# Kernel optimization log

Hardware: AMD Instinct MI355X
Metric: run time of the kernel (lower is better)

## Reference

```python
import jax, jax.numpy as jnp
import numpy as np


def setup_inputs() -> dict:
    key = jax.random.key(0)
    k1, k2 = jax.random.split(key)
    IN, OUT, N = 4096, 4096, 8192
    x = jax.random.normal(k1, (N, IN), dtype=jnp.float32)
    fc = jnp.arange(OUT, dtype=jnp.float32).reshape(-1, 1)  # learned param, init = arange
    bias = jax.random.normal(k2, (OUT,), dtype=jnp.float32) * 0.5
    return {"x": x, "fc": fc, "bias": bias}


def _dst_matrix(fc, in_features, dtype):
    out_features = fc.shape[0]
    t = jnp.arange(in_features, dtype=dtype)[None, :]          # [1, in]
    # torch.eye(out, 1): column vector, 1 at row 0 else 0
    eye_col = jnp.zeros((out_features, 1), dtype=dtype).at[0, 0].set(1.0)
    norm = jax.lax.rsqrt(2.0 * in_features * (eye_col + 1.0))  # [out, 1]
    # dst_m[k, t] = 2 * norm[k] * sin(pi/2 * (k+1)/in * (2t+1))
    dst_m = 2.0 * norm * jnp.sin(0.5 * jnp.pi * ((fc + 1.0) / in_features) * (2.0 * t + 1.0))
    return dst_m  # [out, in]


def reference(x, fc, bias):
    in_features = x.shape[-1]
    w = _dst_matrix(fc, in_features, x.dtype)  # [out, in]
    # F.linear: y = x @ w.T + bias
    return jnp.einsum('ni,oi->no', x, w) + bias
```

## Files before the change

### kernel.cpp

```cpp
#include <hip/hip_runtime.h>
#include <cstdint>
#include <cstddef>

#define IN_F 4096
#define OUT_F 4096
#define NROWS 8192
#define PI_F 3.14159265358979323846f

#define PD(a) ((a) + ((a) >> 4) + 3 * ((a) >> 7))
#define ROWSTR 2224

__device__ inline float2 cmul(float2 a, float2 b) {
    return make_float2(a.x * b.x - a.y * b.y, a.x * b.y + a.y * b.x);
}

__global__ void twprep(float2* __restrict__ tw, float2* __restrict__ f3,
                       float2* __restrict__ f23) {
    const int i = blockIdx.x * 256 + threadIdx.x;
    float s, c;
    if (i < 1024) {
        sincosf(-PI_F * (float)i / 1024.0f, &s, &c);
        tw[i] = make_float2(c, s);
    }
    sincosf(-PI_F * (float)i / 8192.0f, &s, &c);
    f3[i] = make_float2(c, s);
    sincosf(-PI_F * 5.0f * (float)i / 8192.0f, &s, &c);
    f23[i] = make_float2(c, s);
}

struct c4 { float2 z0, z1, z2, z3; };
__device__ __forceinline__ c4 r4unit(float2 x0, float2 x1, float2 x2, float2 x3) {
    const float2 E = make_float2(x0.x + x2.x, x0.y + x2.y);
    const float2 G = make_float2(x0.x - x2.x, x0.y - x2.y);
    const float2 F = make_float2(x1.x + x3.x, x1.y + x3.y);
    const float2 H = make_float2(x1.x - x3.x, x1.y - x3.y);
    c4 r;
    r.z0 = make_float2(E.x + F.x, E.y + F.y);
    r.z2 = make_float2(E.x - F.x, E.y - F.y);
    r.z1 = make_float2(G.x + H.y, G.y - H.x);
    r.z3 = make_float2(G.x - H.y, G.y + H.x);
    return r;
}

template<int S>
__device__ __forceinline__ void dif4(float2* __restrict__ V, int t,
                                     float2 u1, float2 u2) {
    const int h = 512 >> (2 * S);
    const int i = t & (h - 1);
    const int base = ((t >> (9 - 2 * S)) << (11 - 2 * S)) + i;
    const float2 u3 = cmul(u1, u2);
    const int p0 = PD(base), p1 = PD(base + h), p2 = PD(base + 2 * h),
              p3 = PD(base + 3 * h);
    const c4 r = r4unit(V[p0], V[p1], V[p2], V[p3]);
    V[p0] = r.z0;
    V[p1] = cmul(u1, r.z1);
    V[p2] = cmul(u2, r.z2);
    V[p3] = cmul(u3, r.z3);
}

#define WFENCE do { \
    asm volatile("s_waitcnt lgkmcnt(0)" ::: "memory"); \
    __builtin_amdgcn_sched_barrier(0); \
} while (0)

__global__ __launch_bounds__(512, 6) void dst_row(const float* __restrict__ x,
                                                  const float* __restrict__ bias,
                                                  const float2* __restrict__ twg,
                                                  const float2* __restrict__ f3,
                                                  const float2* __restrict__ f23,
                                                  float* __restrict__ out) {
    __shared__ float2 VV[2][ROWSTR];
    const int t = threadIdx.x;
    const int row0 = blockIdx.x * 2;
    const float* xr0 = x + (size_t)row0 * IN_F;
    const float* xr1 = xr0 + IN_F;
    float2* VA = VV[0];
    float2* VB = VV[1];

    const float2 w1 = twg[t];
    const float2 w2 = twg[2 * t];
    const float2 s1u1 = twg[(t & 127) << 2];
    const float2 s1u2 = twg[(t & 127) << 3];
    const float2 s2u1 = twg[(t & 31) << 4];
    const float2 s2u2 = twg[(t & 31) << 5];
    const float2 s3u1 = twg[(t & 7) << 6];
    const float2 s3u2 = twg[(t & 7) << 7];
    const float2 s4u1 = twg[(t & 1) << 8];
    const float2 s4u2 = twg[(t & 1) << 9];

    {
        const float2 w3 = cmul(w1, w2);
        {
            const float4 v0 = *(const float4*)(xr0 + 4 * t);
            const float4 v1 = *(const float4*)(xr0 + 4 * (t + 512));
            const float4 v2 = *(const float4*)(xr0 + (4092 - 4 * t));
            const float4 v3 = *(const float4*)(xr0 + (2044 - 4 * t));
            const c4 r = r4unit(make_float2(v0.x, v0.z), make_float2(v1.x, v1.z),
                                make_float2(-v2.w, -v2.y), make_float2(-v3.w, -v3.y));
            VA[PD(t)]        = r.z0;
            VA[PD(t + 512)]  = cmul(w1, r.z1);
            VA[PD(t + 1024)] = cmul(w2, r.z2);
            VA[PD(t + 1536)] = cmul(w3, r.z3);
        }
        {
            const float4 v0 = *(const float4*)(xr1 + 4 * t);
            const float4 v1 = *(const float4*)(xr1 + 4 * (t + 512));
            const float4 v2 = *(const float4*)(xr1 + (4092 - 4 * t));
            const float4 v3 = *(const float4*)(xr1 + (2044 - 4 * t));
            const c4 r = r4unit(make_float2(v0.x, v0.z), make_float2(v1.x, v1.z),
                                make_float2(-v2.w, -v2.y), make_float2(-v3.w, -v3.y));
            VB[PD(t)]        = r.z0;
            VB[PD(t + 512)]  = cmul(w1, r.z1);
            VB[PD(t + 1024)] = cmul(w2, r.z2);
            VB[PD(t + 1536)] = cmul(w3, r.z3);
        }
    }
    __syncthreads();

    dif4<1>(VA, t, s1u1, s1u2);
    dif4<1>(VB, t, s1u1, s1u2);
    __syncthreads();

    dif4<2>(VA, t, s2u1, s2u2);
    dif4<2>(VB, t, s2u1, s2u2);
    WFENCE;
    dif4<3>(VA, t, s3u1, s3u2);
    dif4<3>(VB, t, s3u1, s3u2);
    WFENCE;
    dif4<4>(VA, t, s4u1, s4u2);
    dif4<4>(VB, t, s4u1, s4u2);
    __syncthreads();

    const int rr = t >> 8;
    const int u = t & 255;
    const float2* V = VV[rr];
    float* yr = out + (size_t)(row0 + rr) * OUT_F;
    const float amp1 = 2.0f * rsqrtf(8192.0f);
    const float amp0 = 2.0f * rsqrtf(16384.0f);
#pragma unroll
    for (int q = 0; q < 8; ++q) {
        const int k = u + (q << 8);
        const int P = ((k & 3) << 9) | (((k >> 2) & 3) << 7) | (((k >> 4) & 3) << 5)
                    | (((k >> 6) & 3) << 3) | (((k >> 8) & 3) << 1);
        const float2 a = V[PD(P)];
        const float2 b = V[PD(P) + 1];
        const float2 z = (k < 1024) ? make_float2(a.x + b.x, a.y + b.y)
                                    : make_float2(a.x - b.x, a.y - b.y);
        const int kc = (2048 - k) & 2047;
        const int Pc = ((kc & 3) << 9) | (((kc >> 2) & 3) << 7) | (((kc >> 4) & 3) << 5)
                     | (((kc >> 6) & 3) << 3) | (((kc >> 8) & 3) << 1);
        const float2 ac = V[PD(Pc)];
        const float2 bc = V[PD(Pc) + 1];
        const float2 zc = (kc < 1024) ? make_float2(ac.x + bc.x, ac.y + bc.y)
                                      : make_float2(ac.x - bc.x, ac.y - bc.y);
        const float Arr = 0.5f * (z.x + zc.x), Aii = 0.5f * (z.y - zc.y);
        const float Brr = 0.5f * (z.y + zc.y), Bii = 0.5f * (zc.x - z.x);
        const float2 e3 = f3[k];
        const float2 eA = f23[k];
        const float Wr = Arr * e3.x - Aii * e3.y + Brr * eA.x - Bii * eA.y;
        const float Wi = Arr * e3.y + Aii * e3.x + Brr * eA.y + Bii * eA.x;
        const int o1 = 4095 - k;
        yr[o1] = amp1 * Wr + bias[o1];
        if (k > 0) {
            const int o2 = k - 1;
            const float amp = (o2 == 0) ? amp0 : amp1;
            yr[o2] = amp * (-Wi) + bias[o2];
        } else {
            const float C2048 = (z.x - z.y) * 0.70710678118654752f;
            yr[2047] = amp1 * C2048 + bias[2047];
        }
    }
}

__global__ __launch_bounds__(256) void dst_row_fb(const float* __restrict__ x,
                                                  const float* __restrict__ bias,
                                                  float* __restrict__ out) {
    __shared__ float Ar[2048], Ai[2048], Br[2048], Bi[2048];
    const int t = threadIdx.x;
    const int row = blockIdx.x;
    const float* xr = x + (size_t)row * IN_F;
    float* yr = out + (size_t)row * OUT_F;
#pragma unroll
    for (int q = 0; q < 8; ++q) {
        const int m = t + q * 256;
        float re, im;
        if (m < 1024) {
            const float4 v = *(const float4*)(xr + 4 * m);
            re = v.x; im = v.z;
        } else {
            const float4 v = *(const float4*)(xr + (8188 - 4 * m));
            re = -v.w; im = -v.y;
        }
        Ar[m] = re; Ai[m] = im;
    }
    __syncthreads();
    float *sr = Ar, *si = Ai, *dr = Br, *di = Bi;
    for (int s = 0; s < 11; ++s) {
        const int mm = 1024 >> s;
#pragma unroll
        for (int q = 0; q < 4; ++q) {
            const int b = t + q * 256;
            const int j = b >> (10 - s);
            const int i = b & (mm - 1);
            const int i0 = i + j * 2 * mm;
            const float ar = sr[i0], aim = si[i0];
            const float cr = sr[i0 + mm], ci = si[i0 + mm];
            float sw, cw;
            __sincosf(-PI_F * (float)j / (float)(1 << s), &sw, &cw);
            const float wr = cr * cw - ci * sw;
            const float wi = cr * sw + ci * cw;
            const int o0 = i + j * mm;
            dr[o0] = ar + wr;        di[o0] = aim + wi;
            dr[o0 + 1024] = ar - wr; di[o0 + 1024] = aim - wi;
        }
        __syncthreads();
        float* tp;
        tp = sr; sr = dr; dr = tp;
        tp = si; si = di; di = tp;
    }
    const float amp1 = 2.0f * rsqrtf(8192.0f);
    const float amp0 = 2.0f * rsqrtf(16384.0f);
#pragma unroll
    for (int q = 0; q < 8; ++q) {
        const int k = t + q * 256;
        const float zr = sr[k], zi = si[k];
        const int kc = (2048 - k) & 2047;
        const float cr = sr[kc], ci = si[kc];
        const float Arr = 0.5f * (zr + cr), Aii = 0.5f * (zi - ci);
        const float Brr = 0.5f * (zi + ci), Bii = 0.5f * (cr - zr);
        float s2, c2;
        __sincosf(-PI_F * (float)k / 2048.0f, &s2, &c2);
        const float Vr = Arr + Brr * c2 - Bii * s2;
        const float Vi = Aii + Brr * s2 + Bii * c2;
        float s3, c3;
        __sincosf(-PI_F * (float)k / 8192.0f, &s3, &c3);
        const float Wr = Vr * c3 - Vi * s3;
        const float Wi = Vr * s3 + Vi * c3;
        const int o1 = 4095 - k;
        yr[o1] = amp1 * Wr + bias[o1];
        if (k > 0) {
            const int o2 = k - 1;
            const float amp = (o2 == 0) ? amp0 : amp1;
            yr[o2] = amp * (-Wi) + bias[o2];
        } else {
            const float C2048 = (zr - zi) * 0.70710678118654752f;
            yr[2047] = amp1 * C2048 + bias[2047];
        }
    }
}

extern "C" void kernel_launch(void* const* d_in, const int* in_sizes, int n_in,
                              void* d_out, int out_size, void* d_ws, size_t ws_size,
                              hipStream_t stream) {
    const float* x    = (const float*)d_in[0];
    const float* bias = (const float*)d_in[2];
    float* out = (float*)d_out;

    if (ws_size >= 40960) {
        float2* tw  = (float2*)d_ws;
        float2* f3  = (float2*)((char*)d_ws + 8192);
        float2* f23 = (float2*)((char*)d_ws + 24576);
        twprep<<<8, 256, 0, stream>>>(tw, f3, f23);
        dst_row<<<NROWS / 2, 512, 0, stream>>>(x, bias, tw, f3, f23, out);
    } else {
        dst_row_fb<<<NROWS, 256, 0, stream>>>(x, bias, out);
    }
}
```

Baseline: 89.65 us.

## Assign one wavefront per row FFT, removing block-wide barriers between stages

Restructures the DST kernel so each 64-lane wavefront handles a whole 4096-point row (4 rows per 256-thread block). Every FFT stage then needs only a wavefront-local LDS wait instead of __syncthreads, and twiddles are staged once per block into shared memory rather than held in registers per thread. Each lane now does 8x more butterflies per stage, which lengthens the serial work per wave and may cut the number of loads in flight per row. It also changes occupancy through new launch bounds and a larger LDS footprint.

```diff
diff --git a/kernel.cpp b/kernel.cpp
--- a/kernel.cpp
+++ b/kernel.cpp
@@ -42,104 +42,88 @@
     return r;
 }
 
-template<int S>
-__device__ __forceinline__ void dif4(float2* __restrict__ V, int t,
-                                     float2 u1, float2 u2) {
-    const int h = 512 >> (2 * S);
-    const int i = t & (h - 1);
-    const int base = ((t >> (9 - 2 * S)) << (11 - 2 * S)) + i;
-    const float2 u3 = cmul(u1, u2);
-    const int p0 = PD(base), p1 = PD(base + h), p2 = PD(base + 2 * h),
-              p3 = PD(base + 3 * h);
-    const c4 r = r4unit(V[p0], V[p1], V[p2], V[p3]);
-    V[p0] = r.z0;
-    V[p1] = cmul(u1, r.z1);
-    V[p2] = cmul(u2, r.z2);
-    V[p3] = cmul(u3, r.z3);
-}
-
 #define WFENCE do { \
     asm volatile("s_waitcnt lgkmcnt(0)" ::: "memory"); \
     __builtin_amdgcn_sched_barrier(0); \
 } while (0)
 
-__global__ __launch_bounds__(512, 6) void dst_row(const float* __restrict__ x,
+template<int S>
+__device__ __forceinline__ void dif4w(float2* __restrict__ V,
+                                      const float2* __restrict__ TW, int lane) {
+#pragma unroll
+    for (int q = 0; q < 8; ++q) {
+        const int b = q * 64 + lane;
+        const int h = 512 >> (2 * S);
+        const int i = b & (h - 1);
+        const int base = ((b >> (9 - 2 * S)) << (11 - 2 * S)) + i;
+        const float2 u1 = TW[i << (2 * S)];
+        const float2 u2 = TW[i << (2 * S + 1)];
+        const float2 u3 = cmul(u1, u2);
+        const int p0 = PD(base), p1 = PD(base + h), p2 = PD(base + 2 * h),
+                  p3 = PD(base + 3 * h);
+        const c4 r = r4unit(V[p0], V[p1], V[p2], V[p3]);
+        V[p0] = r.z0;
+        V[p1] = cmul(u1, r.z1);
+        V[p2] = cmul(u2, r.z2);
+        V[p3] = cmul(u3, r.z3);
+    }
+}
+
+__global__ __launch_bounds__(256, 2) void dst_row(const float* __restrict__ x,
                                                   const float* __restrict__ bias,
                                                   const float2* __restrict__ twg,
                                                   const float2* __restrict__ f3,
                                                   const float2* __restrict__ f23,
                                                   float* __restrict__ out) {
-    __shared__ float2 VV[2][ROWSTR];
+    __shared__ float2 VR[4][ROWSTR];
+    __shared__ float2 TW[1024];
     const int t = threadIdx.x;
-    const int row0 = blockIdx.x * 2;
-    const float* xr0 = x + (size_t)row0 * IN_F;
-    const float* xr1 = xr0 + IN_F;
-    float2* VA = VV[0];
-    float2* VB = VV[1];
-
-    const float2 w1 = twg[t];
-    const float2 w2 = twg[2 * t];
-    const float2 s1u1 = twg[(t & 127) << 2];
-    const float2 s1u2 = twg[(t & 127) << 3];
-    const float2 s2u1 = twg[(t & 31) << 4];
-    const float2 s2u2 = twg[(t & 31) << 5];
-    const float2 s3u1 = twg[(t & 7) << 6];
-    const float2 s3u2 = twg[(t & 7) << 7];
-    const float2 s4u1 = twg[(t & 1) << 8];
-    const float2 s4u2 = twg[(t & 1) << 9];
-
-    {
+    const int lane = t & 63;
+    const int w = t >> 6;
+    const int row = blockIdx.x * 4 + w;
+    const float* xr = x + (size_t)row * IN_F;
+    float* yr = out + (size_t)row * OUT_F;
+    float2* V = VR[w];
+
+    TW[t] = twg[t];
+    TW[t + 256] = twg[t + 256];
+    TW[t + 512] = twg[t + 512];
+    TW[t + 768] = twg[t + 768];
+    __syncthreads();
+
+#pragma unroll
+    for (int q = 0; q < 8; ++q) {
+        const int m = q * 64 + lane;
+        const float4 v0 = *(const float4*)(xr + 4 * m);
+        const float4 v1 = *(const float4*)(xr + 4 * (m + 512));
+        const float4 v2 = *(const float4*)(xr + (4092 - 4 * m));
+        const float4 v3 = *(const float4*)(xr + (2044 - 4 * m));
+        const c4 r = r4unit(make_float2(v0.x, v0.z), make_float2(v1.x, v1.z),
+                            make_float2(-v2.w, -v2.y), make_float2(-v3.w, -v3.y));
+        const float2 w1 = TW[m];
+        const float2 w2 = TW[2 * m];
         const float2 w3 = cmul(w1, w2);
-        {
-            const float4 v0 = *(const float4*)(xr0 + 4 * t);
-            const float4 v1 = *(const float4*)(xr0 + 4 * (t + 512));
-            const float4 v2 = *(const float4*)(xr0 + (4092 - 4 * t));
-            const float4 v3 = *(const float4*)(xr0 + (2044 - 4 * t));
-            const c4 r = r4unit(make_float2(v0.x, v0.z), make_float2(v1.x, v1.z),
-                                make_float2(-v2.w, -v2.y), make_float2(-v3.w, -v3.y));
-            VA[PD(t)]        = r.z0;
-            VA[PD(t + 512)]  = cmul(w1, r.z1);
-            VA[PD(t + 1024)] = cmul(w2, r.z2);
-            VA[PD(t + 1536)] = cmul(w3, r.z3);
-        }
-        {
-            const float4 v0 = *(const float4*)(xr1 + 4 * t);
-            const float4 v1 = *(const float4*)(xr1 + 4 * (t + 512));
-            const float4 v2 = *(const float4*)(xr1 + (4092 - 4 * t));
-            const float4 v3 = *(const float4*)(xr1 + (2044 - 4 * t));
-            const c4 r = r4unit(make_float2(v0.x, v0.z), make_float2(v1.x, v1.z),
-                                make_float2(-v2.w, -v2.y), make_float2(-v3.w, -v3.y));
-            VB[PD(t)]        = r.z0;
-            VB[PD(t + 512)]  = cmul(w1, r.z1);
-            VB[PD(t + 1024)] = cmul(w2, r.z2);
-            VB[PD(t + 1536)] = cmul(w3, r.z3);
-        }
-    }
-    __syncthreads();
-
-    dif4<1>(VA, t, s1u1, s1u2);
-    dif4<1>(VB, t, s1u1, s1u2);
-    __syncthreads();
-
-    dif4<2>(VA, t, s2u1, s2u2);
-    dif4<2>(VB, t, s2u1, s2u2);
-    WFENCE;
-    dif4<3>(VA, t, s3u1, s3u2);
-    dif4<3>(VB, t, s3u1, s3u2);
-    WFENCE;
-    dif4<4>(VA, t, s4u1, s4u2);
-    dif4<4>(VB, t, s4u1, s4u2);
-    __syncthreads();
-
-    const int rr = t >> 8;
-    const int u = t & 255;
-    const float2* V = VV[rr];
-    float* yr = out + (size_t)(row0 + rr) * OUT_F;
+        V[PD(m)]        = r.z0;
+        V[PD(m + 512)]  = cmul(w1, r.z1);
+        V[PD(m + 1024)] = cmul(w2, r.z2);
+        V[PD(m + 1536)] = cmul(w3, r.z3);
+    }
+    WFENCE;
+
+    dif4w<1>(V, TW, lane);
+    WFENCE;
+    dif4w<2>(V, TW, lane);
+    WFENCE;
+    dif4w<3>(V, TW, lane);
+    WFENCE;
+    dif4w<4>(V, TW, lane);
+    WFENCE;
+
     const float amp1 = 2.0f * rsqrtf(8192.0f);
     const float amp0 = 2.0f * rsqrtf(16384.0f);
-#pragma unroll
-    for (int q = 0; q < 8; ++q) {
-        const int k = u + (q << 8);
+#pragma unroll 4
+    for (int q = 0; q < 32; ++q) {
+        const int k = q * 64 + lane;
         const int P = ((k & 3) << 9) | (((k >> 2) & 3) << 7) | (((k >> 4) & 3) << 5)
                     | (((k >> 6) & 3) << 3) | (((k >> 8) & 3) << 1);
         const float2 a = V[PD(P)];
@@ -261,7 +245,7 @@
         float2* f3  = (float2*)((char*)d_ws + 8192);
         float2* f23 = (float2*)((char*)d_ws + 24576);
         twprep<<<8, 256, 0, stream>>>(tw, f3, f23);
-        dst_row<<<NROWS / 2, 512, 0, stream>>>(x, bias, tw, f3, f23, out);
+        dst_row<<<NROWS / 4, 256, 0, stream>>>(x, bias, tw, f3, f23, out);
     } else {
         dst_row_fb<<<NROWS, 256, 0, stream>>>(x, bias, out);
     }
```

After: 105.2 us. +17.4%, slower.
